# Kernel tuning notes

Hardware: AMD Instinct MI355X
Metric: run time of the kernel (lower is better)

The kernel has to match this reference:

```python
import jax, jax.numpy as jnp
import numpy as np

IN_C = 128
OUT_C = 128
MEM = 512
HID = MEM // 2  # 256, per ParameterGenerator hidden_channels = memory_size // 2
T = 8          # number of edge types (keys of edge_feas_dict)
N = 500_000


def setup_inputs() -> dict:
    key = jax.random.key(0)
    ks = jax.random.split(key, 16)
    s = 0.02
    inp = {
        "x": jax.random.normal(ks[0], (N, IN_C), dtype=jnp.float32),
        "type_vec": jax.random.randint(ks[1], (N,), 0, T),
        "edge_feas": jax.random.normal(ks[2], (T, MEM), dtype=jnp.float32),
        # weight_generator MLP: Linear(MEM,HID) -> ReLU -> Linear(HID,HID) -> ReLU -> Linear(HID, IN_C*OUT_C)
        "wg_w1": jax.random.normal(ks[3], (MEM, HID), dtype=jnp.float32) * s,
        "wg_b1": jnp.zeros((HID,), dtype=jnp.float32),
        "wg_w2": jax.random.normal(ks[4], (HID, HID), dtype=jnp.float32) * s,
        "wg_b2": jnp.zeros((HID,), dtype=jnp.float32),
        "wg_w3": jax.random.normal(ks[5], (HID, IN_C * OUT_C), dtype=jnp.float32) * s,
        "wg_b3": jnp.zeros((IN_C * OUT_C,), dtype=jnp.float32),
        # bias_generator MLP: Linear(MEM,HID) -> ReLU -> Linear(HID,HID) -> ReLU -> Linear(HID, OUT_C)
        "bg_w1": jax.random.normal(ks[6], (MEM, HID), dtype=jnp.float32) * s,
        "bg_b1": jnp.zeros((HID,), dtype=jnp.float32),
        "bg_w2": jax.random.normal(ks[7], (HID, HID), dtype=jnp.float32) * s,
        "bg_b2": jnp.zeros((HID,), dtype=jnp.float32),
        "bg_w3": jax.random.normal(ks[8], (HID, OUT_C), dtype=jnp.float32) * s,
        "bg_b3": jnp.zeros((OUT_C,), dtype=jnp.float32),
    }
    return inp


def _mlp(m, w1, b1, w2, b2, w3, b3):
    h = jax.nn.relu(m @ w1 + b1)
    h = jax.nn.relu(h @ w2 + b2)
    return h @ w3 + b3


def reference(x, type_vec, edge_feas,
              wg_w1, wg_b1, wg_w2, wg_b2, wg_w3, wg_b3,
              bg_w1, bg_b1, bg_w2, bg_b2, bg_w3, bg_b3):
    # Generate per-type weights [T, IN_C, OUT_C] and biases [T, OUT_C]
    W = _mlp(edge_feas, wg_w1, wg_b1, wg_w2, wg_b2, wg_w3, wg_b3).reshape(T, IN_C, OUT_C)
    B = _mlp(edge_feas, bg_w1, bg_b1, bg_w2, bg_b2, bg_w3, bg_b3)  # [T, OUT_C]
    # Masked per-type linear, scattered back: out[n] = x[n] @ W[type_vec[n]] + B[type_vec[n]]
    out = jnp.zeros((x.shape[0], OUT_C), dtype=x.dtype)
    for t in range(T):  # small fixed set of types
        yt = x @ W[t] + B[t]
        out = jnp.where((type_vec == t)[:, None], yt, out)
    return out
```

## Files before the change

### kernel.cpp

```cpp
#include <hip/hip_runtime.h>
#include <hip/hip_bf16.h>

#define NT 8
#define MEMC 512
#define HID 256
#define C 128

typedef __attribute__((ext_vector_type(8))) short short8;
typedef __attribute__((ext_vector_type(4))) short short4v;
typedef __attribute__((ext_vector_type(4))) float f32x4;

__device__ inline short f2bf(float f) {
    union { __hip_bfloat16 b; short s; } u;
    u.b = __float2bfloat16(f);
    return u.s;
}

__global__ __launch_bounds__(256) void k1_init_genh(
    const float* __restrict__ edge_feas,
    const float* __restrict__ wg_w1, const float* __restrict__ wg_b1,
    const float* __restrict__ wg_w2, const float* __restrict__ wg_b2,
    const float* __restrict__ bg_w1, const float* __restrict__ bg_b1,
    const float* __restrict__ bg_w2, const float* __restrict__ bg_b2,
    int* __restrict__ hist, int* __restrict__ cursor,
    int* __restrict__ idx, int idx_cap,
    float* __restrict__ h_wg, float* __restrict__ h_bg,
    int n_init_blocks)
{
    int b = blockIdx.x, tid = threadIdx.x;
    if (b < n_init_blocks) {
        int pos = b * 1024 + tid * 4;
        if (pos < idx_cap) *(int4*)(idx + pos) = make_int4(-1, -1, -1, -1);
        return;
    }
    if (b == n_init_blocks) {
        if (tid < NT) { hist[tid] = 0; cursor[tid * 16] = 0; }
        return;
    }
    int gb = b - n_init_blocks - 1;
    int t = gb & 7;
    int gen = gb >> 3;
    const float* w1 = gen ? bg_w1 : wg_w1;
    const float* b1 = gen ? bg_b1 : wg_b1;
    const float* w2 = gen ? bg_w2 : wg_w2;
    const float* b2 = gen ? bg_b2 : wg_b2;
    float* hout = gen ? h_bg : h_wg;

    __shared__ float m[MEMC];
    __shared__ float part[4][HID];
    __shared__ float h1[HID];
    m[tid]       = edge_feas[t * MEMC + tid];
    m[tid + 256] = edge_feas[t * MEMC + tid + 256];
    __syncthreads();

    int w = tid >> 6, l = tid & 63;
    {
        float ax = 0.f, ay = 0.f, az = 0.f, aw = 0.f;
        const float* wp = w1 + (size_t)(w * 128) * HID + 4 * l;
        #pragma unroll 8
        for (int k = 0; k < 128; ++k) {
            float4 v = *(const float4*)(wp + (size_t)k * HID);
            float mk = m[w * 128 + k];
            ax += mk * v.x; ay += mk * v.y; az += mk * v.z; aw += mk * v.w;
        }
        *(float4*)&part[w][4 * l] = make_float4(ax, ay, az, aw);
    }
    __syncthreads();
    {
        float s = part[0][tid] + part[1][tid] + part[2][tid] + part[3][tid] + b1[tid];
        h1[tid] = fmaxf(s, 0.f);
    }
    __syncthreads();
    {
        float ax = 0.f, ay = 0.f, az = 0.f, aw = 0.f;
        const float* wp = w2 + (size_t)(w * 64) * HID + 4 * l;
        #pragma unroll 8
        for (int k = 0; k < 64; ++k) {
            float4 v = *(const float4*)(wp + (size_t)k * HID);
            float hk = h1[w * 64 + k];
            ax += hk * v.x; ay += hk * v.y; az += hk * v.z; aw += hk * v.w;
        }
        *(float4*)&part[w][4 * l] = make_float4(ax, ay, az, aw);
    }
    __syncthreads();
    {
        float s = part[0][tid] + part[1][tid] + part[2][tid] + part[3][tid] + b2[tid];
        hout[t * HID + tid] = fmaxf(s, 0.f);
    }
}

__global__ __launch_bounds__(256) void k2_hist_genw(
    const int* __restrict__ type_vec, int N,
    const float* __restrict__ h_wg, const float* __restrict__ h_bg,
    const float* __restrict__ wg_w3, const float* __restrict__ wg_b3,
    const float* __restrict__ bg_w3, const float* __restrict__ bg_b3,
    int* __restrict__ hist, short* __restrict__ Wkn, float* __restrict__ Bias,
    int n_hist_blocks)
{
    int b = blockIdx.x, tid = threadIdx.x;
    __shared__ float sh[2048];
    __shared__ float sp[2048];
    if (b < n_hist_blocks) {
        __shared__ int lh[NT];
        if (tid < NT) lh[tid] = 0;
        __syncthreads();
        int base = b * 1024 + tid;
        #pragma unroll
        for (int i = 0; i < 4; ++i) {
            int n = base + i * 256;
            if (n < N) atomicAdd(&lh[type_vec[n]], 1);
        }
        __syncthreads();
        if (tid < NT) atomicAdd(&hist[tid], lh[tid]);
        return;
    }
    int gb = b - n_hist_blocks;
    if (gb < 256) {
        for (int i = tid; i < 2048; i += 256) sh[i] = h_wg[i];
        __syncthreads();
        int cl = tid & 63, p = tid >> 6;
        int col = gb * 64 + cl;
        float acc[NT];
        #pragma unroll
        for (int t = 0; t < NT; ++t) acc[t] = 0.f;
        const float* wp = wg_w3 + (size_t)(p * 64) * (C * C) + col;
        #pragma unroll 8
        for (int j = 0; j < 64; ++j) {
            float v = wp[(size_t)j * (C * C)];
            #pragma unroll
            for (int t = 0; t < NT; ++t) acc[t] += sh[t * 256 + p * 64 + j] * v;
        }
        #pragma unroll
        for (int t = 0; t < NT; ++t) sp[p * 512 + t * 64 + cl] = acc[t];
        __syncthreads();
        #pragma unroll
        for (int r = 0; r < 2; ++r) {
            int o = tid + 256 * r;
            int t = o >> 6, c2 = o & 63;
            float s = sp[t * 64 + c2] + sp[512 + t * 64 + c2]
                    + sp[1024 + t * 64 + c2] + sp[1536 + t * 64 + c2]
                    + wg_b3[gb * 64 + c2];
            Wkn[t * (C * C) + gb * 64 + c2] = f2bf(s);
        }
        return;
    }
    for (int i = tid; i < 2048; i += 256) sh[i] = h_bg[i];
    __syncthreads();
    int cl = tid & 127, p = tid >> 7;
    float acc[NT];
    #pragma unroll
    for (int t = 0; t < NT; ++t) acc[t] = 0.f;
    const float* wp = bg_w3 + (size_t)(p * 128) * C + cl;
    #pragma unroll 8
    for (int j = 0; j < 128; ++j) {
        float v = wp[(size_t)j * C];
        #pragma unroll
        for (int t = 0; t < NT; ++t) acc[t] += sh[t * 256 + p * 128 + j] * v;
    }
    #pragma unroll
    for (int t = 0; t < NT; ++t) sp[p * 1024 + t * 128 + cl] = acc[t];
    __syncthreads();
    #pragma unroll
    for (int r = 0; r < 4; ++r) {
        int o = tid + 256 * r;
        int t = o >> 7, c2 = o & 127;
        Bias[t * C + c2] = sp[t * 128 + c2] + sp[1024 + t * 128 + c2] + bg_b3[c2];
    }
}

__global__ __launch_bounds__(256) void k4_scatter_transpose(
    const int* __restrict__ type_vec, int N,
    const int* __restrict__ hist, int* __restrict__ cursor,
    int* __restrict__ idx,
    const short* __restrict__ Wkn, short* __restrict__ Wt,
    int n_scatter_blocks)
{
    int b = blockIdx.x, tid = threadIdx.x;
    if (b >= n_scatter_blocks) {
        int t = b - n_scatter_blocks;
        __shared__ short tile[C][C + 8];
        const short* src = Wkn + t * (C * C);
        for (int i = tid; i < C * C; i += 256)
            tile[i >> 7][i & 127] = src[i];
        __syncthreads();
        short* dst = Wt + t * (C * C);
        for (int i = tid; i < C * C; i += 256)
            dst[i] = tile[i & 127][i >> 7];
        return;
    }
    int seg[NT];
    {
        int s = 0;
        #pragma unroll
        for (int t = 0; t < NT; ++t) { seg[t] = s; s += ((hist[t] + 63) >> 6) << 6; }
    }
    int lane = tid & 63;
    int wave = b * 4 + (tid >> 6);
    int start = wave * 1024;
    if (start >= N) return;

    int cnt[NT];
    #pragma unroll
    for (int t = 0; t < NT; ++t) cnt[t] = 0;
    for (int c = 0; c < 16; ++c) {
        int n = start + c * 64 + lane;
        int mt = (n < N) ? type_vec[n] : NT;
        #pragma unroll
        for (int t = 0; t < NT; ++t)
            cnt[t] += __popcll(__ballot(mt == t));
    }
    int base = 0;
    if (lane < NT) base = atomicAdd(&cursor[lane * 16], cnt[lane]);
    int run[NT];
    #pragma unroll
    for (int t = 0; t < NT; ++t) run[t] = seg[t] + __shfl(base, t, 64);
    unsigned long long below = (1ULL << lane) - 1ULL;
    for (int c = 0; c < 16; ++c) {
        int n = start + c * 64 + lane;
        int mt = (n < N) ? type_vec[n] : NT;
        int mypos = 0;
        #pragma unroll
        for (int t = 0; t < NT; ++t) {
            unsigned long long msk = __ballot(mt == t);
            if (mt == t) mypos = run[t] + __popcll(msk & below);
            run[t] += __popcll(msk);
        }
        if (n < N) idx[mypos] = n;
    }
}

#define AS_LD 136
#define BS_LD 136
#define CS_LD 132

__global__ __launch_bounds__(256, 3) void k5_gemm(
    const float* __restrict__ x, const int* __restrict__ idx,
    const short* __restrict__ Wt, const float* __restrict__ Bias,
    const int* __restrict__ hist, float* __restrict__ out)
{
    __shared__ __align__(16) char smem[64 * AS_LD * 2 + 128 * BS_LD * 2];
    short (*As)[AS_LD] = (short(*)[AS_LD])smem;
    short (*Bs)[BS_LD] = (short(*)[BS_LD])(smem + 64 * AS_LD * 2);
    float (*Cs)[CS_LD] = (float(*)[CS_LD])(smem + 64 * AS_LD * 2);
    __shared__ int ridx[64];

    int tid = threadIdx.x;
    int lane = tid & 63, w = tid >> 6;
    int block_base = blockIdx.x * 64;

    int seg[NT + 1];
    {
        int s = 0;
        #pragma unroll
        for (int t = 0; t < NT; ++t) { seg[t] = s; s += ((hist[t] + 63) >> 6) << 6; }
        seg[NT] = s;
    }
    if (block_base >= seg[NT]) return;
    int t = 0;
    #pragma unroll
    for (int i = 1; i < NT; ++i)
        if (block_base >= seg[i]) t = i;

    if (tid < 64) ridx[tid] = idx[block_base + tid];
    __syncthreads();

    {
        int rbase = 16 * w + (lane >> 5);
        int c4 = (lane & 31) * 4;
        #pragma unroll
        for (int i = 0; i < 8; ++i) {
            int r = rbase + i * 2;
            int node = ridx[r];
            float4 v = make_float4(0.f, 0.f, 0.f, 0.f);
            if (node >= 0) v = *(const float4*)(x + (size_t)node * C + c4);
            short4v sv;
            sv[0] = f2bf(v.x); sv[1] = f2bf(v.y);
            sv[2] = f2bf(v.z); sv[3] = f2bf(v.w);
            *(short4v*)&As[r][c4] = sv;
        }
    }
    {
        int rr = w * 32 + (lane >> 4);
        int c8 = (lane & 15) * 8;
        const short* src = Wt + t * (C * C);
        #pragma unroll
        for (int i = 0; i < 8; ++i) {
            int r = rr + i * 4;
            short8 v = *(const short8*)(src + r * C + c8);
            *(short8*)&Bs[r][c8] = v;
        }
    }
    __syncthreads();

    int quad = lane >> 4, m16 = lane & 15;
    float bv[8];
    #pragma unroll
    for (int ni = 0; ni < 8; ++ni) bv[ni] = Bias[t * C + ni * 16 + m16];

    f32x4 acc[8];
    #pragma unroll
    for (int i = 0; i < 8; ++i) acc[i] = (f32x4){0.f, 0.f, 0.f, 0.f};

    #pragma unroll
    for (int kk = 0; kk < 4; ++kk) {
        short8 af = *(const short8*)&As[16 * w + m16][kk * 32 + quad * 8];
        #pragma unroll
        for (int ni = 0; ni < 8; ++ni) {
            short8 bf = *(const short8*)&Bs[ni * 16 + m16][kk * 32 + quad * 8];
            acc[ni] = __builtin_amdgcn_mfma_f32_16x16x32_bf16(af, bf, acc[ni], 0, 0, 0);
        }
    }
    __syncthreads();

    #pragma unroll
    for (int ni = 0; ni < 8; ++ni) {
        int colc = ni * 16 + m16;
        #pragma unroll
        for (int r = 0; r < 4; ++r)
            Cs[16 * w + quad * 4 + r][colc] = acc[ni][r] + bv[ni];
    }
    __syncthreads();

    {
        int rbase = 16 * w + (lane >> 5);
        int c4 = (lane & 31) * 4;
        #pragma unroll
        for (int i = 0; i < 8; ++i) {
            int r = rbase + i * 2;
            int node = ridx[r];
            if (node >= 0) {
                float4 v = *(const float4*)&Cs[r][c4];
                *(float4*)(out + (size_t)node * C + c4) = v;
            }
        }
    }
}

extern "C" void kernel_launch(void* const* d_in, const int* in_sizes, int n_in,
                              void* d_out, int out_size, void* d_ws, size_t ws_size,
                              hipStream_t stream)
{
    const float* x         = (const float*)d_in[0];
    const int*   type_vec  = (const int*)d_in[1];
    const float* edge_feas = (const float*)d_in[2];
    const float* wg_w1 = (const float*)d_in[3];
    const float* wg_b1 = (const float*)d_in[4];
    const float* wg_w2 = (const float*)d_in[5];
    const float* wg_b2 = (const float*)d_in[6];
    const float* wg_w3 = (const float*)d_in[7];
    const float* wg_b3 = (const float*)d_in[8];
    const float* bg_w1 = (const float*)d_in[9];
    const float* bg_b1 = (const float*)d_in[10];
    const float* bg_w2 = (const float*)d_in[11];
    const float* bg_b2 = (const float*)d_in[12];
    const float* bg_w3 = (const float*)d_in[13];
    const float* bg_b3 = (const float*)d_in[14];
    float* out = (float*)d_out;
    int N = in_sizes[1];

    char* ws = (char*)d_ws;
    int*   hist   = (int*)(ws + 0);
    int*   cursor = (int*)(ws + 128);
    float* h_wg   = (float*)(ws + 1024);
    float* h_bg   = (float*)(ws + 9216);
    float* Bias   = (float*)(ws + 17408);
    short* Wkn    = (short*)(ws + 21504);
    short* Wt     = (short*)(ws + 283648);
    int*   idx    = (int*)(ws + 545792);

    int nblk64  = (N + 63) / 64;
    int idx_cap = (nblk64 + 8) * 64;
    int n_init  = (idx_cap + 1023) / 1024;
    int n_hist  = (N + 1023) / 1024;
    int n_scat  = (n_hist + 3) / 4;

    k1_init_genh<<<n_init + 17, 256, 0, stream>>>(
        edge_feas, wg_w1, wg_b1, wg_w2, wg_b2, bg_w1, bg_b1, bg_w2, bg_b2,
        hist, cursor, idx, idx_cap, h_wg, h_bg, n_init);

    k2_hist_genw<<<n_hist + 257, 256, 0, stream>>>(
        type_vec, N, h_wg, h_bg, wg_w3, wg_b3, bg_w3, bg_b3,
        hist, Wkn, Bias, n_hist);

    k4_scatter_transpose<<<n_scat + 8, 256, 0, stream>>>(
        type_vec, N, hist, cursor, idx, Wkn, Wt, n_scat);

    k5_gemm<<<nblk64 + 8, 256, 0, stream>>>(x, idx, Wt, Bias, hist, out);
}
```

Measured before the change: 546.1 us.

## Drop LDS staging in grouped GEMM; load fragments directly from global

The per-type GEMM kernel no longer stages x, W and the output tile through shared memory. Each lane loads its A fragment straight from the gathered x rows, reads B fragments directly from global (cache-resident) weights, and writes results with scalar stores to scattered output rows. Occupancy hint raised from 3 to 4 blocks. This removes barriers and LDS traffic but makes output stores 4-byte, 16-lane-coalesced (64B segments) instead of float4 rows, and increases redundant global/L2 reads of W.

```diff
diff --git a/kernel.cpp b/kernel.cpp
--- a/kernel.cpp
+++ b/kernel.cpp
@@ -229,23 +229,14 @@
     }
 }
 
-#define AS_LD 136
-#define BS_LD 136
-#define CS_LD 132
-
-__global__ __launch_bounds__(256, 3) void k5_gemm(
+__global__ __launch_bounds__(256, 4) void k5_gemm(
     const float* __restrict__ x, const int* __restrict__ idx,
     const short* __restrict__ Wt, const float* __restrict__ Bias,
     const int* __restrict__ hist, float* __restrict__ out)
 {
-    __shared__ __align__(16) char smem[64 * AS_LD * 2 + 128 * BS_LD * 2];
-    short (*As)[AS_LD] = (short(*)[AS_LD])smem;
-    short (*Bs)[BS_LD] = (short(*)[BS_LD])(smem + 64 * AS_LD * 2);
-    float (*Cs)[CS_LD] = (float(*)[CS_LD])(smem + 64 * AS_LD * 2);
-    __shared__ int ridx[64];
-
     int tid = threadIdx.x;
     int lane = tid & 63, w = tid >> 6;
+    int m16 = lane & 15, quad = lane >> 4;
     int block_base = blockIdx.x * 64;
 
     int seg[NT + 1];
@@ -261,77 +252,55 @@
     for (int i = 1; i < NT; ++i)
         if (block_base >= seg[i]) t = i;
 
-    if (tid < 64) ridx[tid] = idx[block_base + tid];
-    __syncthreads();
-
-    {
-        int rbase = 16 * w + (lane >> 5);
-        int c4 = (lane & 31) * 4;
-        #pragma unroll
-        for (int i = 0; i < 8; ++i) {
-            int r = rbase + i * 2;
-            int node = ridx[r];
-            float4 v = make_float4(0.f, 0.f, 0.f, 0.f);
-            if (node >= 0) v = *(const float4*)(x + (size_t)node * C + c4);
-            short4v sv;
-            sv[0] = f2bf(v.x); sv[1] = f2bf(v.y);
-            sv[2] = f2bf(v.z); sv[3] = f2bf(v.w);
-            *(short4v*)&As[r][c4] = sv;
-        }
-    }
-    {
-        int rr = w * 32 + (lane >> 4);
-        int c8 = (lane & 15) * 8;
-        const short* src = Wt + t * (C * C);
-        #pragma unroll
-        for (int i = 0; i < 8; ++i) {
-            int r = rr + i * 4;
-            short8 v = *(const short8*)(src + r * C + c8);
-            *(short8*)&Bs[r][c8] = v;
-        }
-    }
-    __syncthreads();
-
-    int quad = lane >> 4, m16 = lane & 15;
-    float bv[8];
-    #pragma unroll
-    for (int ni = 0; ni < 8; ++ni) bv[ni] = Bias[t * C + ni * 16 + m16];
+    int row0 = block_base + 16 * w;
+    int node_a = idx[row0 + m16];
+
+    short8 af[4];
+    {
+        const float* xr = x + (size_t)(node_a < 0 ? 0 : node_a) * C + quad * 8;
+        #pragma unroll
+        for (int kk = 0; kk < 4; ++kk) {
+            float4 v0 = *(const float4*)(xr + kk * 32);
+            float4 v1 = *(const float4*)(xr + kk * 32 + 4);
+            short8 sv;
+            sv[0] = f2bf(v0.x); sv[1] = f2bf(v0.y);
+            sv[2] = f2bf(v0.z); sv[3] = f2bf(v0.w);
+            sv[4] = f2bf(v1.x); sv[5] = f2bf(v1.y);
+            sv[6] = f2bf(v1.z); sv[7] = f2bf(v1.w);
+            af[kk] = sv;
+        }
+        if (node_a < 0) {
+            #pragma unroll
+            for (int kk = 0; kk < 4; ++kk)
+                af[kk] = (short8){0, 0, 0, 0, 0, 0, 0, 0};
+        }
+    }
 
     f32x4 acc[8];
     #pragma unroll
     for (int i = 0; i < 8; ++i) acc[i] = (f32x4){0.f, 0.f, 0.f, 0.f};
 
+    const short* bw = Wt + t * (C * C) + m16 * C + quad * 8;
     #pragma unroll
     for (int kk = 0; kk < 4; ++kk) {
-        short8 af = *(const short8*)&As[16 * w + m16][kk * 32 + quad * 8];
         #pragma unroll
         for (int ni = 0; ni < 8; ++ni) {
-            short8 bf = *(const short8*)&Bs[ni * 16 + m16][kk * 32 + quad * 8];
-            acc[ni] = __builtin_amdgcn_mfma_f32_16x16x32_bf16(af, bf, acc[ni], 0, 0, 0);
-        }
-    }
-    __syncthreads();
+            short8 bf = *(const short8*)(bw + (size_t)ni * 16 * C + kk * 32);
+            acc[ni] = __builtin_amdgcn_mfma_f32_16x16x32_bf16(af[kk], bf, acc[ni], 0, 0, 0);
+        }
+    }
+
+    int node_c[4];
+    #pragma unroll
+    for (int r = 0; r < 4; ++r) node_c[r] = idx[row0 + quad * 4 + r];
 
     #pragma unroll
     for (int ni = 0; ni < 8; ++ni) {
-        int colc = ni * 16 + m16;
-        #pragma unroll
-        for (int r = 0; r < 4; ++r)
-            Cs[16 * w + quad * 4 + r][colc] = acc[ni][r] + bv[ni];
-    }
-    __syncthreads();
-
-    {
-        int rbase = 16 * w + (lane >> 5);
-        int c4 = (lane & 31) * 4;
-        #pragma unroll
-        for (int i = 0; i < 8; ++i) {
-            int r = rbase + i * 2;
-            int node = ridx[r];
-            if (node >= 0) {
-                float4 v = *(const float4*)&Cs[r][c4];
-                *(float4*)(out + (size_t)node * C + c4) = v;
-            }
+        float bv = Bias[t * C + ni * 16 + m16];
+        #pragma unroll
+        for (int r = 0; r < 4; ++r) {
+            if (node_c[r] >= 0)
+                out[(size_t)node_c[r] * C + ni * 16 + m16] = acc[ni][r] + bv;
         }
     }
 }
```

Result: slower. 615.4 us (+12.7%).
